# Kernel tuning notes

Hardware: AMD Instinct MI355X
Metric: run time of the kernel (lower is better)

The kernel has to match this reference:

```python
import itertools
import jax, jax.numpy as jnp
import numpy as np


def _interpn_linear(vol, loc):
    """Trilinear sampling with edge-clamping (voxelmorph interpn, fill_value=None).
    vol: [D, H, W, C] float; loc: [D, H, W, 3] float absolute sample coordinates (ij indexing).
    """
    spatial = vol.shape[:-1]
    ndims = len(spatial)
    maxs = jnp.asarray([s - 1 for s in spatial], dtype=loc.dtype)
    cloc = jnp.clip(loc, 0.0, maxs)             # clamp = nearest-neighbor fill outside domain
    loc0 = jnp.floor(cloc)
    loc1 = jnp.minimum(loc0 + 1.0, maxs)
    d1 = loc1 - cloc                            # weight for the low corner (loc0)
    d0 = 1.0 - d1                               # weight for the high corner (loc1)
    loc0i = loc0.astype(jnp.int32)
    loc1i = loc1.astype(jnp.int32)

    # flatten volume and build per-dim strides for linear indexing
    volf = vol.reshape(-1, vol.shape[-1])       # [D*H*W, C]
    strides = np.ones(ndims, dtype=np.int32)
    for d in range(ndims - 2, -1, -1):
        strides[d] = strides[d + 1] * spatial[d + 1]

    out = jnp.zeros(spatial + (vol.shape[-1],), dtype=vol.dtype)
    for corner in itertools.product((0, 1), repeat=ndims):
        idx = jnp.zeros(spatial, dtype=jnp.int32)
        w = jnp.ones(spatial, dtype=vol.dtype)
        for d in range(ndims):
            idx = idx + (loc1i if corner[d] else loc0i)[..., d] * strides[d]
            w = w * (d0 if corner[d] else d1)[..., d]
        out = out + w[..., None] * jnp.take(volf, idx, axis=0)
    return out


def _warp_single(vol, disp):
    """Apply dense displacement field: sample vol at identity grid + disp."""
    spatial = vol.shape[:-1]
    grid = jnp.stack(
        jnp.meshgrid(*[jnp.arange(s, dtype=disp.dtype) for s in spatial], indexing='ij'),
        axis=-1)                                # [D, H, W, 3]
    return _interpn_linear(vol, grid + disp)


def setup_inputs() -> dict:
    key = jax.random.key(0)
    k1, k2 = jax.random.split(key)
    vol = jax.random.normal(k1, (2, 128, 192, 192, 1), dtype=jnp.float32)
    trf = jax.random.normal(k2, (2, 128, 192, 192, 3), dtype=jnp.float32)
    return {"vol": vol, "trf": trf}


def reference(vol, trf):
    # batched dense-warp spatial transformer (single_transform=False)
    return jax.vmap(_warp_single)(vol, trf)
```

## Files before the change

kernel.cpp:

```cpp
#include <hip/hip_runtime.h>
#include <stdint.h>


#define BD 128
#define BH 192
#define BW 192
#define DHW (BD*BH*BW)
#define NB 2

#define TX 16
#define TY 8
#define NTX (BW/TX)
#define NTY (BH/TY)
#define NZB 4
#define NSTEPB 4
#define NBLK (NTX*NTY*NZB*NB)
#define NXCD 8

#define SXW 32
#define SYW 16
#define SLAB (SXW*SYW)
#define RING 24
#define LDSF (RING*SLAB)

typedef float f4v __attribute__((ext_vector_type(4)));

__device__ __forceinline__ int mod24(int z) {
    return (int)((unsigned)z % 24u);
}

__global__ __launch_bounds__(256, 3) void st_warp_kernel(
    const float* __restrict__ vol,
    const float* __restrict__ trf,
    float* __restrict__ out)
{
    __shared__ __align__(16) float lds[LDSF];

    const int bid = blockIdx.x;
    const int swz = (bid % NXCD) * (NBLK / NXCD) + bid / NXCD;
    int t = swz;
    const int txi = t % NTX; t /= NTX;
    const int tyi = t % NTY; t /= NTY;
    const int kzb = t % NZB; t /= NZB;
    const int b   = t;
    const int tx = txi*TX, ty = tyi*TY;
    const int zA = kzb * (NSTEPB*8);

    const int sx = min(max(tx - 8, 0), BW - SXW);
    const int sy = min(max(ty - 4, 0), BH - SYW);

    const int tid = (int)threadIdx.x;
    const float* volb = vol + (size_t)b * DHW;

    const int xq = tid & 3;
    const int yb = (tid >> 2) & 7;
    const int zb = tid >> 5;
    const int Y  = ty + yb;
    const int Xb = tx + xq*4;
    const f4v* trf4 = (const f4v*)trf;

    auto stage = [&](int zfirst, int nslab) {
        const int nch = nslab << 7;
        for (int it = 0; it*256 < nch; ++it) {
            const int f = tid + it*256;
            if (f < nch) {
                const int z  = zfirst + (f >> 7);
                const int s  = f & 127;
                const int yi = s >> 3;
                const int c  = s & 7;
                const int slot = mod24(z);
                const float* g = volb + ((size_t)(z*BH + sy + yi))*BW + sx + (c<<2);
                __builtin_amdgcn_global_load_lds(
                    (const __attribute__((address_space(1))) void*)g,
                    (__attribute__((address_space(3))) void*)&lds[(slot<<9) + (s<<2)],
                    16, 0, 0);
            }
        }
    };

    auto load_trf = [&](int ZS, f4v& TA, f4v& TB, f4v& TC) {
        const size_t rowf4 = ((size_t)((b*BD + ZS + zb)*BH + Y)*BW + tx) * 3 / 4;
        TA = trf4[rowf4 + 3*xq + 0];
        TB = trf4[rowf4 + 3*xq + 1];
        TC = trf4[rowf4 + 3*xq + 2];
    };

    auto compute = [&](int ZS, f4v tA, f4v tB, f4v tC) {
        const int Z   = ZS + zb;
        const int wlo = max(0, ZS - 4);
        const int whi = min(BD - 1, ZS + 11);
        const float dzs[4] = {tA.x, tA.w, tB.z, tC.y};
        const float dys[4] = {tA.y, tB.x, tB.w, tC.z};
        const float dxs[4] = {tA.z, tB.y, tC.x, tC.w};
        float res[4];
#pragma unroll
        for (int jj = 0; jj < 4; ++jj) {
            float cz = fminf(fmaxf((float)Z + dzs[jj], 0.f), (float)(BD-1));
            float cy = fminf(fmaxf((float)Y + dys[jj], 0.f), (float)(BH-1));
            float cx = fminf(fmaxf((float)(Xb+jj) + dxs[jj], 0.f), (float)(BW-1));
            float fz = floorf(cz), fy = floorf(cy), fx = floorf(cx);
            int z0 = (int)fz, y0 = (int)fy, x0 = (int)fx;
            int z1 = min(z0+1, BD-1);
            int y1 = min(y0+1, BH-1);
            int x1 = min(x0+1, BW-1);
            float wz = cz - fz, wy = cy - fy, wx = cx - fx;
            float v000,v001,v010,v011,v100,v101,v110,v111;
            bool inwin = (x0 >= sx) & (x1 <= sx+SXW-1) & (y0 >= sy) & (y1 <= sy+SYW-1)
                       & (z0 >= wlo) & (z1 <= whi);
            if (inwin) {
                const int xi  = x0 - sx;
                const int xiA = min(xi, SXW-2);
                const bool lo = xi < SXW-1;
                int sl0 = mod24(z0);
                int sl1 = sl0 + 1;
                sl1 = (sl1 == RING) ? 0 : sl1;
                sl1 = (z1 == z0) ? sl0 : sl1;
                const int yt0 = (y0 - sy) << 5, yt1 = (y1 - sy) << 5;
                const int rA = (sl0<<9) + yt0 + xiA;
                const int rB = (sl0<<9) + yt1 + xiA;
                const int rC = (sl1<<9) + yt0 + xiA;
                const int rD = (sl1<<9) + yt1 + xiA;
                float a00 = lds[rA], b00 = lds[rA+1];
                float a01 = lds[rB], b01 = lds[rB+1];
                float a10 = lds[rC], b10 = lds[rC+1];
                float a11 = lds[rD], b11 = lds[rD+1];
                v000 = lo ? a00 : b00;  v001 = b00;
                v010 = lo ? a01 : b01;  v011 = b01;
                v100 = lo ? a10 : b10;  v101 = b10;
                v110 = lo ? a11 : b11;  v111 = b11;
            } else {
                const float* p00 = volb + ((size_t)z0*BH + y0)*BW;
                const float* p01 = volb + ((size_t)z0*BH + y1)*BW;
                const float* p10 = volb + ((size_t)z1*BH + y0)*BW;
                const float* p11 = volb + ((size_t)z1*BH + y1)*BW;
                v000 = p00[x0]; v001 = p00[x1];
                v010 = p01[x0]; v011 = p01[x1];
                v100 = p10[x0]; v101 = p10[x1];
                v110 = p11[x0]; v111 = p11[x1];
            }
            float c00 = v000 + wx*(v001-v000);
            float c01 = v010 + wx*(v011-v010);
            float c10 = v100 + wx*(v101-v100);
            float c11 = v110 + wx*(v111-v110);
            float c0  = c00 + wy*(c01-c00);
            float c1  = c10 + wy*(c11-c10);
            res[jj]   = c0 + wz*(c1-c0);
        }
        f4v r = {res[0], res[1], res[2], res[3]};
        const size_t of4 = ((size_t)((b*BD + Z)*BH + Y)*BW + Xb) / 4;
        __builtin_nontemporal_store(r, &((f4v*)out)[of4]);
    };

    f4v A0,B0,C0, A1,B1,C1;
    stage(max(0, zA - 4), (zA == 0) ? 12 : 16);
    load_trf(zA, A0, B0, C0);
    __syncthreads();

#pragma unroll
    for (int kk = 0; kk < NSTEPB; kk += 2) {
        {
            const int zc = zA + kk*8;
            const int zn = zc + 12;
            if (zn < BD) stage(zn, min(8, BD - zn));
            load_trf(zc + 8, A1, B1, C1);
            compute(zc, A0, B0, C0);
            __syncthreads();
        }
        {
            const int zc = zA + kk*8 + 8;
            const int zn = zc + 12;
            if (kk + 2 < NSTEPB && zn < BD) stage(zn, min(8, BD - zn));
            if (kk + 2 < NSTEPB) load_trf(zc + 8, A0, B0, C0);
            compute(zc, A1, B1, C1);
            __syncthreads();
        }
    }
}

extern "C" void kernel_launch(void* const* d_in, const int* in_sizes, int n_in,
                              void* d_out, int out_size, void* d_ws, size_t ws_size,
                              hipStream_t stream) {
    const float* vol = (const float*)d_in[0];
    const float* trf = (const float*)d_in[1];
    float* out = (float*)d_out;

    st_warp_kernel<<<dim3(NBLK), dim3(256), 0, stream>>>(vol, trf, out);
}
```

Measured before the change: 42.62 us.

## Reshape warp tile to 16x16 rows with 4-slice z steps and power-of-two ring

The block tile grows from 16x8 to 16x16 in y and the z step shrinks from 8 to 4 slices. The LDS window is now 32x24 with a 16-slot ring indexed by a bit mask instead of a modulo by 24. The aim is less halo staging per output, since the y halo is shared across more rows and each step stages 4 new slices. The lower clamp at 0 is dropped and replaced by clamping indices only on the global fallback path, which trims ALU work. The z window is narrower (+7 instead of +11), so more samples may miss LDS and fall back to scattered global loads.

```diff
diff --git a/kernel.cpp b/kernel.cpp
--- a/kernel.cpp
+++ b/kernel.cpp
@@ -9,25 +9,24 @@
 #define NB 2
 
 #define TX 16
-#define TY 8
+#define TY 16
 #define NTX (BW/TX)
 #define NTY (BH/TY)
-#define NZB 4
+#define ZSTEP 4
 #define NSTEPB 4
+#define BLKZ (ZSTEP*NSTEPB)
+#define NZB (BD/BLKZ)
 #define NBLK (NTX*NTY*NZB*NB)
 #define NXCD 8
 
 #define SXW 32
-#define SYW 16
+#define SYW 24
 #define SLAB (SXW*SYW)
-#define RING 24
+#define CHSLAB (SLAB/4)
+#define RING 16
 #define LDSF (RING*SLAB)
 
 typedef float f4v __attribute__((ext_vector_type(4)));
-
-__device__ __forceinline__ int mod24(int z) {
-    return (int)((unsigned)z % 24u);
-}
 
 __global__ __launch_bounds__(256, 3) void st_warp_kernel(
     const float* __restrict__ vol,
@@ -44,7 +43,7 @@
     const int kzb = t % NZB; t /= NZB;
     const int b   = t;
     const int tx = txi*TX, ty = tyi*TY;
-    const int zA = kzb * (NSTEPB*8);
+    const int zA = kzb * BLKZ;
 
     const int sx = min(max(tx - 8, 0), BW - SXW);
     const int sy = min(max(ty - 4, 0), BH - SYW);
@@ -53,51 +52,51 @@
     const float* volb = vol + (size_t)b * DHW;
 
     const int xq = tid & 3;
-    const int yb = (tid >> 2) & 7;
-    const int zb = tid >> 5;
+    const int yb = (tid >> 2) & 15;
+    const int zb = tid >> 6;
     const int Y  = ty + yb;
     const int Xb = tx + xq*4;
     const f4v* trf4 = (const f4v*)trf;
 
     auto stage = [&](int zfirst, int nslab) {
-        const int nch = nslab << 7;
-        for (int it = 0; it*256 < nch; ++it) {
-            const int f = tid + it*256;
-            if (f < nch) {
-                const int z  = zfirst + (f >> 7);
-                const int s  = f & 127;
-                const int yi = s >> 3;
-                const int c  = s & 7;
-                const int slot = mod24(z);
-                const float* g = volb + ((size_t)(z*BH + sy + yi))*BW + sx + (c<<2);
-                __builtin_amdgcn_global_load_lds(
-                    (const __attribute__((address_space(1))) void*)g,
-                    (__attribute__((address_space(3))) void*)&lds[(slot<<9) + (s<<2)],
-                    16, 0, 0);
-            }
+        const int iters = (nslab * CHSLAB) >> 8;
+        for (int it = 0; it < iters; ++it) {
+            const int f  = tid + it*256;
+            const int sl = (int)((unsigned)f / (unsigned)CHSLAB);
+            const int s  = f - sl*CHSLAB;
+            const int z  = zfirst + sl;
+            const int yi = s >> 3;
+            const int c  = s & 7;
+            const int slot = z & (RING-1);
+            const float* g = volb + ((size_t)(z*BH + sy + yi))*BW + sx + (c<<2);
+            __builtin_amdgcn_global_load_lds(
+                (const __attribute__((address_space(1))) void*)g,
+                (__attribute__((address_space(3))) void*)&lds[slot*SLAB + (s<<2)],
+                16, 0, 0);
         }
     };
 
-    auto load_trf = [&](int ZS, f4v& TA, f4v& TB, f4v& TC) {
-        const size_t rowf4 = ((size_t)((b*BD + ZS + zb)*BH + Y)*BW + tx) * 3 / 4;
+    auto load_trf = [&](int ZSL, f4v& TA, f4v& TB, f4v& TC) {
+        const size_t rowb = ((size_t)((b*BD + ZSL + zb)*BH + Y))*BW;
+        const size_t rowf4 = (rowb + tx) * 3 / 4;
         TA = trf4[rowf4 + 3*xq + 0];
         TB = trf4[rowf4 + 3*xq + 1];
         TC = trf4[rowf4 + 3*xq + 2];
     };
 
-    auto compute = [&](int ZS, f4v tA, f4v tB, f4v tC) {
+    auto compute_vals = [&](int ZS, f4v tA, f4v tB, f4v tC) -> f4v {
         const int Z   = ZS + zb;
         const int wlo = max(0, ZS - 4);
-        const int whi = min(BD - 1, ZS + 11);
+        const int whi = min(BD - 1, ZS + 7);
         const float dzs[4] = {tA.x, tA.w, tB.z, tC.y};
         const float dys[4] = {tA.y, tB.x, tB.w, tC.z};
         const float dxs[4] = {tA.z, tB.y, tC.x, tC.w};
         float res[4];
 #pragma unroll
         for (int jj = 0; jj < 4; ++jj) {
-            float cz = fminf(fmaxf((float)Z + dzs[jj], 0.f), (float)(BD-1));
-            float cy = fminf(fmaxf((float)Y + dys[jj], 0.f), (float)(BH-1));
-            float cx = fminf(fmaxf((float)(Xb+jj) + dxs[jj], 0.f), (float)(BW-1));
+            float cz = fminf((float)Z + dzs[jj], (float)(BD-1));
+            float cy = fminf((float)Y + dys[jj], (float)(BH-1));
+            float cx = fminf((float)(Xb+jj) + dxs[jj], (float)(BW-1));
             float fz = floorf(cz), fy = floorf(cy), fx = floorf(cx);
             int z0 = (int)fz, y0 = (int)fy, x0 = (int)fx;
             int z1 = min(z0+1, BD-1);
@@ -111,15 +110,13 @@
                 const int xi  = x0 - sx;
                 const int xiA = min(xi, SXW-2);
                 const bool lo = xi < SXW-1;
-                int sl0 = mod24(z0);
-                int sl1 = sl0 + 1;
-                sl1 = (sl1 == RING) ? 0 : sl1;
-                sl1 = (z1 == z0) ? sl0 : sl1;
-                const int yt0 = (y0 - sy) << 5, yt1 = (y1 - sy) << 5;
-                const int rA = (sl0<<9) + yt0 + xiA;
-                const int rB = (sl0<<9) + yt1 + xiA;
-                const int rC = (sl1<<9) + yt0 + xiA;
-                const int rD = (sl1<<9) + yt1 + xiA;
+                const int sl0 = z0 & (RING-1);
+                const int sl1 = z1 & (RING-1);
+                const int yi0 = y0 - sy, yi1 = y1 - sy;
+                const int rA = sl0*SLAB + (yi0<<5) + xiA;
+                const int rB = sl0*SLAB + (yi1<<5) + xiA;
+                const int rC = sl1*SLAB + (yi0<<5) + xiA;
+                const int rD = sl1*SLAB + (yi1<<5) + xiA;
                 float a00 = lds[rA], b00 = lds[rA+1];
                 float a01 = lds[rB], b01 = lds[rB+1];
                 float a10 = lds[rC], b10 = lds[rC+1];
@@ -129,14 +126,17 @@
                 v100 = lo ? a10 : b10;  v101 = b10;
                 v110 = lo ? a11 : b11;  v111 = b11;
             } else {
-                const float* p00 = volb + ((size_t)z0*BH + y0)*BW;
-                const float* p01 = volb + ((size_t)z0*BH + y1)*BW;
-                const float* p10 = volb + ((size_t)z1*BH + y0)*BW;
-                const float* p11 = volb + ((size_t)z1*BH + y1)*BW;
-                v000 = p00[x0]; v001 = p00[x1];
-                v010 = p01[x0]; v011 = p01[x1];
-                v100 = p10[x0]; v101 = p10[x1];
-                v110 = p11[x0]; v111 = p11[x1];
+                const int z0c = max(z0, 0), z1c = max(z1, 0);
+                const int y0c = max(y0, 0), y1c = max(y1, 0);
+                const int x0c = max(x0, 0), x1c = max(x1, 0);
+                const float* p00 = volb + ((size_t)z0c*BH + y0c)*BW;
+                const float* p01 = volb + ((size_t)z0c*BH + y1c)*BW;
+                const float* p10 = volb + ((size_t)z1c*BH + y0c)*BW;
+                const float* p11 = volb + ((size_t)z1c*BH + y1c)*BW;
+                v000 = p00[x0c]; v001 = p00[x1c];
+                v010 = p01[x0c]; v011 = p01[x1c];
+                v100 = p10[x0c]; v101 = p10[x1c];
+                v110 = p11[x0c]; v111 = p11[x1c];
             }
             float c00 = v000 + wx*(v001-v000);
             float c01 = v010 + wx*(v011-v010);
@@ -147,33 +147,26 @@
             res[jj]   = c0 + wz*(c1-c0);
         }
         f4v r = {res[0], res[1], res[2], res[3]};
-        const size_t of4 = ((size_t)((b*BD + Z)*BH + Y)*BW + Xb) / 4;
-        __builtin_nontemporal_store(r, &((f4v*)out)[of4]);
+        return r;
     };
 
-    f4v A0,B0,C0, A1,B1,C1;
-    stage(max(0, zA - 4), (zA == 0) ? 12 : 16);
-    load_trf(zA, A0, B0, C0);
+    f4v TA[2], TB[2], TC[2];
+    stage(max(0, zA - 4), (zA == 0) ? 8 : 12);
+    load_trf(zA, TA[0], TB[0], TC[0]);
     __syncthreads();
 
 #pragma unroll
-    for (int kk = 0; kk < NSTEPB; kk += 2) {
-        {
-            const int zc = zA + kk*8;
-            const int zn = zc + 12;
-            if (zn < BD) stage(zn, min(8, BD - zn));
-            load_trf(zc + 8, A1, B1, C1);
-            compute(zc, A0, B0, C0);
-            __syncthreads();
+    for (int k = 0; k < NSTEPB; ++k) {
+        const int ZS = zA + k*ZSTEP;
+        if (k + 1 < NSTEPB) {
+            const int zn = ZS + 8;
+            if (zn < BD) stage(zn, min(4, BD - zn));
+            load_trf(ZS + ZSTEP, TA[(k+1)&1], TB[(k+1)&1], TC[(k+1)&1]);
         }
-        {
-            const int zc = zA + kk*8 + 8;
-            const int zn = zc + 12;
-            if (kk + 2 < NSTEPB && zn < BD) stage(zn, min(8, BD - zn));
-            if (kk + 2 < NSTEPB) load_trf(zc + 8, A0, B0, C0);
-            compute(zc, A1, B1, C1);
-            __syncthreads();
-        }
+        f4v r = compute_vals(ZS, TA[k&1], TB[k&1], TC[k&1]);
+        __syncthreads();
+        const size_t of4 = (((size_t)((b*BD + ZS + zb)*BH + Y))*BW + Xb) / 4;
+        __builtin_nontemporal_store(r, &((f4v*)out)[of4]);
     }
 }
 
```

Measured after the change: 45.50 us. 6.8% more time.
